# Kernel optimization log

Measured on AMD Instinct MI355X. Metric: run time of the kernel, lower is better.

Reference implementation:

```python
import jax, jax.numpy as jnp
import numpy as np

G = 8          # groups
PATCH = 4      # encoder patch conv kernel/stride
MD = 4         # correlation max displacement -> (2*MD+1)^2 = 81 neighbours
BNEPS = 1e-5
LNEPS = 1e-5

# finite-difference gradient kernel (assumed: forward differences on a C-grid)
GRAD_K = jnp.array([[[[0., 0., 0.], [0., -1., 1.], [0., 0., 0.]]],
                    [[[0., 0., 0.], [0., -1., 0.], [0., 1., 0.]]]], dtype=jnp.float32)

def _vort_kernel():
    # assumed 6x6 Biot-Savart-like vorticity->velocity kernel (CalculusOperators not in source)
    c = 2.5
    ys, xs = np.mgrid[0:6, 0:6].astype(np.float32)
    r2 = (ys - c) ** 2 + (xs - c) ** 2
    u = -(ys - c) / (2.0 * np.pi * r2)
    v = (xs - c) / (2.0 * np.pi * r2)
    return jnp.asarray(np.stack([u, v])[:, None])  # [2,1,6,6]
VORT_K = _vort_kernel()

def conv2d(x, w, pad, stride=1):
    return jax.lax.conv_general_dilated(x, w, (stride, stride), [(pad, pad), (pad, pad)],
                                        dimension_numbers=('NCHW', 'OIHW', 'NCHW'))

def bn(x, g, b):
    # inference-mode BatchNorm with running_mean=0, running_var=1
    return x * (g / jnp.sqrt(1.0 + BNEPS))[None, :, None, None] + b[None, :, None, None]

def up2x(x):
    def lerp_axis(x, axis):
        n = x.shape[axis]
        c = jnp.arange(2 * n, dtype=x.dtype) * (n - 1) / (2 * n - 1)
        i0 = jnp.floor(c).astype(jnp.int32)
        i1 = jnp.minimum(i0 + 1, n - 1)
        w = c - i0.astype(x.dtype)
        a0 = jnp.take(x, i0, axis=axis)
        a1 = jnp.take(x, i1, axis=axis)
        shp = [1] * x.ndim; shp[axis] = 2 * n
        w = w.reshape(shp)
        return a0 * (1 - w) + a1 * w
    return lerp_axis(lerp_axis(x, 2), 3)

def double_conv_up(x, w1, g1, b1, w2, g2, b2):
    x = jax.nn.relu(bn(conv2d(up2x(x), w1, 1), g1, b1))
    return jax.nn.relu(bn(conv2d(up2x(x), w2, 1), g2, b2))

@jax.checkpoint
def correlation(f1, f2):
    # PWC-Net style FunctionCorrelation: mean over channels of f1 * shifted f2, 81 shifts
    N, C, H, W = f1.shape
    f2p = jnp.pad(f2, ((0, 0), (0, 0), (MD, MD), (MD, MD)))
    outs = [jnp.mean(f1 * f2p[:, :, dy:dy + H, dx:dx + W], axis=1)
            for dy in range(2 * MD + 1) for dx in range(2 * MD + 1)]
    return jnp.stack(outs, axis=1)  # [N, 81, H, W]

def cgrid_to_motion(u, v, shape):
    mu = (u[:, :, 1:-1, 1:] + u[:, :, 1:-1, :-1]) * 0.5
    mv = (v[:, :, 1:, 1:-1] + v[:, :, :-1, 1:-1]) * 0.5
    m = jnp.concatenate([mu, mv], axis=1)
    h, w = shape
    up = (m.shape[2] - h) // 2
    left = (m.shape[3] - w) // 2
    return m[:, :, up:up + h, left:left + w]

def calc_phi_velocity(phi, shape):
    vel = conv2d(phi, GRAD_K, 1)
    return cgrid_to_motion(vel[:, 0:1, :, :-1], vel[:, 1:2, :-1, :], shape)

def calc_vort_velocity(stream, shape):
    s = stream[:, :, :-1, :-1]
    vel = conv2d(s, VORT_K, 5)  # full-padding conv == conv_transpose of flipped kernel
    return cgrid_to_motion(vel[:, 0:1, 2:-2, 2:-3], vel[:, 1:2, 2:-3, 2:-2], shape)

def bilinear_sample(f, px, py):
    # f [N,C,H,W]; px,py [N,H,W] absolute coords, border clamp
    H, W = f.shape[-2], f.shape[-1]
    px = jnp.clip(px, 0.0, W - 1.0)
    py = jnp.clip(py, 0.0, H - 1.0)
    x0 = jnp.floor(px); y0 = jnp.floor(py)
    wx = (px - x0)[:, None]; wy = (py - y0)[:, None]
    x0i = x0.astype(jnp.int32); y0i = y0.astype(jnp.int32)
    x1i = jnp.minimum(x0i + 1, W - 1); y1i = jnp.minimum(y0i + 1, H - 1)
    gat = jax.vmap(lambda fi, yi, xi: fi[:, yi, xi])
    v00 = gat(f, y0i, x0i); v01 = gat(f, y0i, x1i)
    v10 = gat(f, y1i, x0i); v11 = gat(f, y1i, x1i)
    return (v00 * (1 - wx) + v01 * wx) * (1 - wy) + (v10 * (1 - wx) + v11 * wx) * wy

def warp(f, vel, sign):
    N, _, H, W = f.shape
    ys, xs = jnp.meshgrid(jnp.arange(H, dtype=f.dtype), jnp.arange(W, dtype=f.dtype), indexing='ij')
    return bilinear_sample(f, xs[None] - sign * vel[:, 0], ys[None] - sign * vel[:, 1])

def bfecc_warp(f, vel):
    f1 = warp(f, vel, 1.0)
    fb = warp(f1, vel, -1.0)
    return warp(f + 0.5 * (f - fb), vel, 1.0)

def _forward(prev, next, texture, mask, boundary,
             enc_w, enc_b,
             phi_w1, phi_g1, phi_b1, phi_w2, phi_g2, phi_b2, phi_ow, phi_ob,
             vor_w1, vor_g1, vor_b1, vor_w2, vor_g2, vor_b2, vor_ow, vor_ob,
             phi_weight, vorticity_weight,
             ln_g, ln_b, fc1_w, fc1_b, fc2_w, fc2_b):
    B, C, H, W = prev.shape
    shape = texture.shape[-2:]
    pm = (prev * mask[:, None]).reshape(B * G, C // G, H, W)
    pb = (prev * boundary[:, None]).reshape(B * G, C // G, H, W)
    nm = (next * mask[:, None]).reshape(B * G, C // G, H, W)
    enc = lambda x: conv2d(x, enc_w, 0, PATCH) + enc_b[None, :, None, None]
    f_nm = enc(nm)
    corr = jnp.concatenate([correlation(enc(pm), f_nm), correlation(enc(pb), f_nm)], axis=1)
    phi = (conv2d(double_conv_up(corr, phi_w1, phi_g1, phi_b1, phi_w2, phi_g2, phi_b2), phi_ow, 0)
           + phi_ob[None, :, None, None]) * phi_weight
    vort = (conv2d(double_conv_up(corr, vor_w1, vor_g1, vor_b1, vor_w2, vor_g2, vor_b2), vor_ow, 0)
            + vor_ob[None, :, None, None]) * vorticity_weight * H
    helm = jnp.concatenate([phi, vort], axis=1)  # [B*G, 2, H, W]
    vel_phi = calc_phi_velocity(helm[:, 0:1], shape)
    vel_vort = calc_vort_velocity(helm[:, 1:2], shape)
    vel = vel_phi + vel_vort
    Bt, Ct, Ht, Wt = texture.shape
    tex = texture.reshape(B * G, Ct // G, Ht, Wt)
    pred = bfecc_warp(tex, vel).reshape(B, Ct, Ht, Wt)
    xp = jnp.transpose(pred, (0, 2, 3, 1))  # [B,H,W,C]
    mu = jnp.mean(xp, -1, keepdims=True)
    var = jnp.var(xp, -1, keepdims=True)
    y = (xp - mu) / jnp.sqrt(var + LNEPS) * ln_g + ln_b
    y = jax.nn.gelu(y @ fc1_w.T + fc1_b, approximate=False)
    y = y @ fc2_w.T + fc2_b
    return pred + jnp.transpose(y, (0, 3, 1, 2))

def setup_inputs():
    ks = jax.random.split(jax.random.key(0), 20)
    B, C, H, W = 4, 64, 260, 260
    Ht, Wt = 258, 258
    D = 128           # correlation_dim
    cg = C // G       # 8 channels per group
    ed = 8            # encoder_dim // groups = 64 // 8
    n = lambda i, shp, s=1.0: jax.random.normal(ks[i], shp, jnp.float32) * s
    return {
        'prev': n(0, (B, C, H, W)), 'next': n(1, (B, C, H, W)),
        'texture': n(2, (B, C, Ht, Wt)),
        'mask': jax.random.uniform(ks[3], (B, H, W), jnp.float32),
        'boundary': jax.random.uniform(ks[4], (B, H, W), jnp.float32),
        'enc_w': n(5, (D, cg, PATCH, PATCH), 0.05), 'enc_b': n(6, (D,), 0.02),
        'phi_w1': n(7, (ed, 162, 3, 3), 0.05), 'phi_g1': jnp.ones(ed), 'phi_b1': jnp.zeros(ed),
        'phi_w2': n(8, (ed, ed, 3, 3), 0.05), 'phi_g2': jnp.ones(ed), 'phi_b2': jnp.zeros(ed),
        'phi_ow': n(9, (1, ed, 1, 1), 0.05), 'phi_ob': n(10, (1,), 0.02),
        'vor_w1': n(11, (ed, 162, 3, 3), 0.05), 'vor_g1': jnp.ones(ed), 'vor_b1': jnp.zeros(ed),
        'vor_w2': n(12, (ed, ed, 3, 3), 0.05), 'vor_g2': jnp.ones(ed), 'vor_b2': jnp.zeros(ed),
        'vor_ow': n(13, (1, ed, 1, 1), 0.05), 'vor_ob': n(14, (1,), 0.02),
        'phi_weight': jnp.array([0.5], jnp.float32),
        'vorticity_weight': jnp.array([0.005], jnp.float32),
        'ln_g': jnp.ones(C), 'ln_b': jnp.zeros(C),
        'fc1_w': n(15, (C, C), 0.05), 'fc1_b': n(16, (C,), 0.02),
        'fc2_w': n(17, (C, C), 0.05), 'fc2_b': n(18, (C,), 0.02),
    }

def reference(prev, next, texture, mask, boundary,
              enc_w, enc_b,
              phi_w1, phi_g1, phi_b1, phi_w2, phi_g2, phi_b2, phi_ow, phi_ob,
              vor_w1, vor_g1, vor_b1, vor_w2, vor_g2, vor_b2, vor_ow, vor_ob,
              phi_weight, vorticity_weight,
              ln_g, ln_b, fc1_w, fc1_b, fc2_w, fc2_b):
    return _forward(prev, next, texture, mask, boundary,
                    enc_w, enc_b,
                    phi_w1, phi_g1, phi_b1, phi_w2, phi_g2, phi_b2, phi_ow, phi_ob,
                    vor_w1, vor_g1, vor_b1, vor_w2, vor_g2, vor_b2, vor_ow, vor_ob,
                    phi_weight, vorticity_weight,
                    ln_g, ln_b, fc1_w, fc1_b, fc2_w, fc2_b)
```

## Files before the change

kernel.cpp:

```cpp
#include <hip/hip_runtime.h>
#include <math.h>


#define NIMG 32
#define HW 260
#define HWT 258
#define EG 65
#define EGP (EG*EG)
#define PIX_T (HWT*HWT)
#define PIX_H (HW*HW)
#define H1N 8652800

__global__ void k_wt(const float* __restrict__ w, float* __restrict__ wt) {
    int e = blockIdx.x * 256 + threadIdx.x;
    if (e < 128 * 128) {
        int d = e >> 7, i = e & 127;
        wt[i * 128 + d] = w[e];
    }
}

__global__ __launch_bounds__(128) void k_enc(
    const float* __restrict__ src,
    const float* __restrict__ mul,
    const float* __restrict__ wt,
    const float* __restrict__ bias,
    float* __restrict__ out)
{
    int xt = blockIdx.x;
    int yo = blockIdx.y;
    int n  = blockIdx.z;
    int bi = n >> 3, g = n & 7;
    int xo0 = xt * 16;
    __shared__ __align__(16) float patch[2048];
    int tid = threadIdx.x;
    const float* sbase = src + (size_t)(bi * 64 + g * 8) * PIX_H;
    const float* mbase = mul + (size_t)bi * PIX_H;
    int row0 = yo * 4, col0 = xo0 * 4;
    for (int e = tid; e < 2048; e += 128) {
        int c = e >> 8, r = (e >> 6) & 3, col = e & 63;
        int gc = col0 + col;
        float v = 0.f;
        if (gc < HW) {
            int off = (row0 + r) * HW + gc;
            v = sbase[(size_t)c * PIX_H + off] * mbase[off];
        }
        patch[e] = v;
    }
    __syncthreads();
    int d = tid;
    float acc[16];
    float bv = bias[d];
#pragma unroll
    for (int p = 0; p < 16; ++p) acc[p] = bv;
    const float4* p4 = (const float4*)patch;
    for (int j = 0; j < 32; ++j) {
        float w0 = wt[(j * 4 + 0) * 128 + d];
        float w1 = wt[(j * 4 + 1) * 128 + d];
        float w2 = wt[(j * 4 + 2) * 128 + d];
        float w3 = wt[(j * 4 + 3) * 128 + d];
#pragma unroll
        for (int p = 0; p < 16; ++p) {
            float4 v = p4[j * 16 + p];
            acc[p] += w0 * v.x + w1 * v.y + w2 * v.z + w3 * v.w;
        }
    }
    size_t ob = ((size_t)(n * EG + yo) * EG + xo0) * 128 + d;
#pragma unroll
    for (int p = 0; p < 16; ++p)
        if (xo0 + p < EG) out[ob + (size_t)p * 128] = acc[p];
}

__global__ __launch_bounds__(128) void k_corr(
    const float* __restrict__ f1,
    const float* __restrict__ f2,
    float* __restrict__ corr,
    int obase)
{
    int bx = blockIdx.x;
    int dy = bx >> 1, xt = bx & 1;
    int y  = blockIdx.y;
    int n  = blockIdx.z;
    int xs = xt ? 33 : 0;
    int nx = xt ? 32 : 33;
    __shared__ __align__(16) float4 s1[33 * 17];
    __shared__ __align__(16) float4 s2[41 * 17];
    int tid = threadIdx.x;
    const float4* g1 = (const float4*)(f1 + ((size_t)(n * EG + y) * EG + xs) * 128);
    int y2 = y + dy - 4;
    bool yok = (y2 >= 0 && y2 < EG);
    const float4* g2 = (const float4*)(f2 + (yok ? ((size_t)(n * EG + y2) * EG) * 128 : 0));
    int q, xl;
    if (xt) { q = tid >> 5; xl = tid & 31; }
    else    { q = tid / 33; xl = tid - q * 33; }
    int dx0 = q * 3;
    bool act = tid < nx * 3;
    float4 a0 = make_float4(0,0,0,0), a1 = a0, a2 = a0;
    for (int half = 0; half < 2; ++half) {
        int cb = half * 16;
        __syncthreads();
        for (int e = tid; e < nx * 16; e += 128) {
            int r = e >> 4, c4 = e & 15;
            s1[r * 17 + c4] = g1[r * 32 + cb + c4];
        }
        for (int e = tid; e < 41 * 16; e += 128) {
            int r = e >> 4, c4 = e & 15;
            int xg = xs - 4 + r;
            float4 v = make_float4(0.f, 0.f, 0.f, 0.f);
            if (yok && xg >= 0 && xg < EG) v = g2[xg * 32 + cb + c4];
            s2[r * 17 + c4] = v;
        }
        __syncthreads();
        if (act) {
            const float4* r1 = s1 + xl * 17;
            const float4* r2 = s2 + (xl + dx0) * 17;
#pragma unroll 8
            for (int i = 0; i < 16; ++i) {
                float4 a = r1[i];
                float4 b0 = r2[i], b1 = r2[17 + i], b2 = r2[34 + i];
                a0.x += a.x * b0.x; a0.y += a.y * b0.y; a0.z += a.z * b0.z; a0.w += a.w * b0.w;
                a1.x += a.x * b1.x; a1.y += a.y * b1.y; a1.z += a.z * b1.z; a1.w += a.w * b1.w;
                a2.x += a.x * b2.x; a2.y += a.y * b2.y; a2.z += a.z * b2.z; a2.w += a.w * b2.w;
            }
        }
    }
    if (act) {
        float s[3];
        s[0] = (a0.x + a0.y + a0.z + a0.w) * (1.0f / 128.0f);
        s[1] = (a1.x + a1.y + a1.z + a1.w) * (1.0f / 128.0f);
        s[2] = (a2.x + a2.y + a2.z + a2.w) * (1.0f / 128.0f);
#pragma unroll
        for (int m = 0; m < 3; ++m) {
            int o = obase + dy * 9 + dx0 + m;
            corr[(size_t)(n * 162 + o) * EGP + y * EG + xs + xl] = s[m];
        }
    }
}

__global__ __launch_bounds__(256) void k_conv1(
    const float* __restrict__ corr,
    const float* __restrict__ w_phi,
    const float* __restrict__ w_vor,
    float* __restrict__ part)
{
    int yp = blockIdx.x;
    int n  = blockIdx.y;
    int zp = blockIdx.z;
    int y0 = yp * 4;
    __shared__ float upc[6 * 6 * 132];
    __shared__ float wch[16 * 6 * 9];
    __shared__ float s_xw[132];
    __shared__ int   s_xi0[132];
    __shared__ int   s_xi1[132];
    __shared__ float s_yw[6];
    __shared__ int   s_yj0[6];
    __shared__ int   s_yj1[6];
    __shared__ int   s_yv[6];
    int tid = threadIdx.x;
    if (tid < 132) {
        int xu = tid - 1;
        if (xu >= 0 && xu <= 129) {
            float cx = (float)(xu * 64) / 129.0f;
            int i0 = (int)cx;
            int i1 = i0 + 1; if (i1 > 64) i1 = 64;
            s_xw[tid] = cx - (float)i0;
            s_xi0[tid] = i0;
            s_xi1[tid] = i1;
        } else { s_xi0[tid] = -1; s_xi1[tid] = 0; s_xw[tid] = 0.f; }
    }
    if (tid >= 132 && tid < 138) {
        int r = tid - 132;
        int yy = y0 - 1 + r;
        if (yy >= 0 && yy <= 129) {
            float cy = (float)(yy * 64) / 129.0f;
            int i0 = (int)cy;
            int i1 = i0 + 1; if (i1 > 64) i1 = 64;
            s_yw[r] = cy - (float)i0;
            s_yj0[r] = i0;
            s_yj1[r] = i1;
            s_yv[r] = 1;
        } else { s_yw[r] = 0.f; s_yj0[r] = 0; s_yj1[r] = 0; s_yv[r] = 0; }
    }
    int og = tid / 26, xg = tid - og * 26;
    int x0 = xg * 5;
    bool act = (og < 8);
    float acc[2][4][5] = {};
    for (int cc = zp * 9; cc < zp * 9 + 9; ++cc) {
        int cb = cc * 6;
        __syncthreads();
        for (int e = tid; e < 4752; e += 256) {
            int r = e / 792, rem = e - r * 792, ci = rem / 132, xx = rem - ci * 132;
            float val = 0.f;
            int xi0 = s_xi0[xx];
            if (s_yv[r] && xi0 >= 0) {
                const float* cp = corr + (size_t)(n * 162 + cb + ci) * EGP;
                int J0 = s_yj0[r] * 65, J1 = s_yj1[r] * 65;
                int xi1 = s_xi1[xx];
                float wxv = s_xw[xx];
                float a0 = __ldg(cp + J0 + xi0), a1 = __ldg(cp + J0 + xi1);
                float b0 = __ldg(cp + J1 + xi0), b1 = __ldg(cp + J1 + xi1);
                float tp = a0 + wxv * (a1 - a0);
                float bt = b0 + wxv * (b1 - b0);
                val = tp + s_yw[r] * (bt - tp);
            }
            upc[e] = val;
        }
        for (int e = tid; e < 864; e += 256) {
            int oc = e / 54, rem = e - oc * 54, ci = rem / 9, k = rem - ci * 9;
            int t2 = oc >> 3, o = oc & 7;
            wch[e] = (t2 ? w_vor : w_phi)[(o * 162 + cb + ci) * 9 + k];
        }
        __syncthreads();
        if (act) {
            for (int ci = 0; ci < 6; ++ci) {
                float wr[2][9];
#pragma unroll
                for (int p = 0; p < 2; ++p)
#pragma unroll
                    for (int k = 0; k < 9; ++k)
                        wr[p][k] = wch[((og + 8 * p) * 6 + ci) * 9 + k];
#pragma unroll
                for (int r = 0; r < 6; ++r) {
                    float u7[7];
                    const float* up = &upc[(r * 6 + ci) * 132 + x0];
#pragma unroll
                    for (int m = 0; m < 7; ++m) u7[m] = up[m];
#pragma unroll
                    for (int ky = 0; ky < 3; ++ky) {
                        int yi = r - ky;
                        if (yi < 0 || yi > 3) continue;
#pragma unroll
                        for (int p = 0; p < 2; ++p)
#pragma unroll
                            for (int kx = 0; kx < 3; ++kx) {
                                float w = wr[p][ky * 3 + kx];
#pragma unroll
                                for (int xi = 0; xi < 5; ++xi)
                                    acc[p][yi][xi] += w * u7[xi + kx];
                            }
                    }
                }
            }
        }
    }
    if (act) {
        float* pbuf = part + (size_t)zp * H1N;
#pragma unroll
        for (int p = 0; p < 2; ++p) {
            size_t pb = (size_t)((p * 32 + n) * 8 + og) * 16900;
#pragma unroll
            for (int yi = 0; yi < 4; ++yi) {
                int row = y0 + yi;
                if (row < 130) {
#pragma unroll
                    for (int xi = 0; xi < 5; ++xi)
                        pbuf[pb + (size_t)row * 130 + (x0 + xi)] = acc[p][yi][xi];
                }
            }
        }
    }
}

__global__ __launch_bounds__(256) void k_h1red(
    const float* __restrict__ part,
    const float* __restrict__ g_phi, const float* __restrict__ b_phi,
    const float* __restrict__ g_vor, const float* __restrict__ b_vor,
    float* __restrict__ h1)
{
    int i4 = blockIdx.x * 256 + threadIdx.x;
    if (i4 >= H1N / 4) return;
    size_t i = (size_t)i4 * 4;
    int c2 = (int)(i / 16900);
    int o = c2 & 7, t2 = c2 >> 8;
    const float bnsc = 1.0f / sqrtf(1.0f + 1e-5f);
    float gsc = (t2 ? g_vor[o] : g_phi[o]) * bnsc;
    float bia = (t2 ? b_vor[o] : b_phi[o]);
    const float4* p0 = (const float4*)(part);
    const float4* p1 = (const float4*)(part + H1N);
    const float4* p2 = (const float4*)(part + 2 * (size_t)H1N);
    float4 a = p0[i4], b = p1[i4], c = p2[i4];
    float4 r;
    r.x = fmaxf((a.x + b.x + c.x) * gsc + bia, 0.f);
    r.y = fmaxf((a.y + b.y + c.y) * gsc + bia, 0.f);
    r.z = fmaxf((a.z + b.z + c.z) * gsc + bia, 0.f);
    r.w = fmaxf((a.w + b.w + c.w) * gsc + bia, 0.f);
    ((float4*)h1)[i4] = r;
}

__global__ __launch_bounds__(256) void k_conv2(
    const float* __restrict__ h1,
    const float* __restrict__ w_phi2, const float* __restrict__ w_vor2,
    const float* __restrict__ g_phi2, const float* __restrict__ b_phi2,
    const float* __restrict__ g_vor2, const float* __restrict__ b_vor2,
    const float* __restrict__ ow_phi, const float* __restrict__ ob_phi,
    const float* __restrict__ ow_vor, const float* __restrict__ ob_vor,
    const float* __restrict__ phi_weight, const float* __restrict__ vort_weight,
    float* __restrict__ helm)
{
    int y = blockIdx.x, n = blockIdx.y;
    __shared__ float hraw[8320];
    __shared__ float wch[1152];
    __shared__ float bns[16], bnb[16], owv[16], obv[2], wm[2];
    int tid = threadIdx.x;
    int ylo = y - 1; if (ylo < 0) ylo = 0;
    int R0 = (int)((float)(ylo * 129) / 259.0f);
    for (int e = tid; e < 8320; e += 256) {
        int t2 = e / 4160, rem = e - t2 * 4160;
        int j = rem / 1040, rem2 = rem - j * 1040;
        int ci = rem2 / 130, xx = rem2 - ci * 130;
        int R = R0 + j; if (R > 129) R = 129;
        hraw[e] = h1[(size_t)((t2 * 32 + n) * 8 + ci) * 16900 + R * 130 + xx];
    }
    for (int e = tid; e < 1152; e += 256) {
        int t2 = e / 576, rem = e - t2 * 576;
        int o = rem / 72, rem2 = rem - o * 72;
        int ci = rem2 / 9, k = rem2 - ci * 9;
        wch[e] = (t2 ? w_vor2 : w_phi2)[(o * 8 + ci) * 9 + k];
    }
    if (tid < 16) {
        int t2 = tid >> 3, o = tid & 7;
        bns[tid] = (t2 ? g_vor2[o] : g_phi2[o]) * (1.0f / sqrtf(1.0f + 1e-5f));
        bnb[tid] = (t2 ? b_vor2[o] : b_phi2[o]);
        owv[tid] = (t2 ? ow_vor[o] : ow_phi[o]);
    }
    if (tid == 0) {
        obv[0] = ob_phi[0]; obv[1] = ob_vor[0];
        wm[0] = phi_weight[0]; wm[1] = vort_weight[0] * 260.0f;
    }
    __syncthreads();
    for (int x = tid; x < HW; x += 256) {
        float wy[3]; int rj0[3], rj1[3]; bool vy[3];
#pragma unroll
        for (int ky = 0; ky < 3; ++ky) {
            int yy = y - 1 + ky;
            vy[ky] = (yy >= 0 && yy < HW);
            if (vy[ky]) {
                float cy = (float)(yy * 129) / 259.0f;
                int i0 = (int)cy; wy[ky] = cy - (float)i0;
                int i1 = i0 + 1; if (i1 > 129) i1 = 129;
                rj0[ky] = i0 - R0; rj1[ky] = i1 - R0;
            } else { wy[ky] = 0; rj0[ky] = 0; rj1[ky] = 0; }
        }
        float wxv[3]; int c0[3], c1[3]; bool vx[3];
#pragma unroll
        for (int kx = 0; kx < 3; ++kx) {
            int xxp = x - 1 + kx;
            vx[kx] = (xxp >= 0 && xxp < HW);
            if (vx[kx]) {
                float cx = (float)(xxp * 129) / 259.0f;
                int i0 = (int)cx; wxv[kx] = cx - (float)i0;
                int i1 = i0 + 1; if (i1 > 129) i1 = 129;
                c0[kx] = i0; c1[kx] = i1;
            } else { wxv[kx] = 0; c0[kx] = 0; c1[kx] = 0; }
        }
        float res[2];
#pragma unroll
        for (int t2 = 0; t2 < 2; ++t2) {
            float acc[8] = {0,0,0,0,0,0,0,0};
            for (int ci = 0; ci < 8; ++ci) {
#pragma unroll
                for (int ky = 0; ky < 3; ++ky) {
                    if (!vy[ky]) continue;
                    const float* r0p = &hraw[((t2 * 4 + rj0[ky]) * 8 + ci) * 130];
                    const float* r1p = &hraw[((t2 * 4 + rj1[ky]) * 8 + ci) * 130];
                    float u3[3];
#pragma unroll
                    for (int kx = 0; kx < 3; ++kx) {
                        if (vx[kx]) {
                            float tp = r0p[c0[kx]] + wxv[kx] * (r0p[c1[kx]] - r0p[c0[kx]]);
                            float bt = r1p[c0[kx]] + wxv[kx] * (r1p[c1[kx]] - r1p[c0[kx]]);
                            u3[kx] = tp + wy[ky] * (bt - tp);
                        } else u3[kx] = 0.f;
                    }
#pragma unroll
                    for (int o = 0; o < 8; ++o) {
                        const float* wp = &wch[((t2 * 8 + o) * 8 + ci) * 9 + ky * 3];
                        acc[o] += wp[0] * u3[0] + wp[1] * u3[1] + wp[2] * u3[2];
                    }
                }
            }
            float dot = 0.f;
#pragma unroll
            for (int o = 0; o < 8; ++o) {
                float hv = fmaxf(acc[o] * bns[t2 * 8 + o] + bnb[t2 * 8 + o], 0.f);
                dot += owv[t2 * 8 + o] * hv;
            }
            res[t2] = (dot + obv[t2]) * wm[t2];
        }
        helm[(size_t)(n * 2 + 0) * PIX_H + y * HW + x] = res[0];
        helm[(size_t)(n * 2 + 1) * PIX_H + y * HW + x] = res[1];
    }
}

__device__ __forceinline__ float K0f(int a, int b) {
    if (a < 0 || a > 5 || b < 0 || b > 5) return 0.f;
    float fa = (float)a - 2.5f, fb = (float)b - 2.5f;
    float r2 = fa * fa + fb * fb;
    return -fa / (6.28318530717958647692f * r2);
}
__device__ __forceinline__ float K1f(int a, int b) {
    if (a < 0 || a > 5 || b < 0 || b > 5) return 0.f;
    float fa = (float)a - 2.5f, fb = (float)b - 2.5f;
    float r2 = fa * fa + fb * fb;
    return fb / (6.28318530717958647692f * r2);
}

__global__ __launch_bounds__(256) void k_vel(
    const float* __restrict__ helm, float* __restrict__ vel)
{
    int idx = blockIdx.x * 256 + threadIdx.x;
    if (idx >= NIMG * PIX_T) return;
    int n = idx / PIX_T, pix = idx - n * PIX_T;
    int yy = pix / HWT, xx = pix - yy * HWT;
    const float* phi = helm + (size_t)(n * 2) * PIX_H;
    const float* s   = helm + (size_t)(n * 2 + 1) * PIX_H;
    float sv[7][7];
#pragma unroll
    for (int di = 0; di < 7; ++di) {
        int i = yy + di - 3;
#pragma unroll
        for (int dj = 0; dj < 7; ++dj) {
            int j = xx + dj - 3;
            sv[di][dj] = (i >= 0 && i < 259 && j >= 0 && j < 259) ? s[i * HW + j] : 0.f;
        }
    }
    float ax = 0.5f * (phi[(yy + 1) * HW + xx + 2] - phi[(yy + 1) * HW + xx]);
#pragma unroll
    for (int a = 0; a < 6; ++a)
#pragma unroll
        for (int d = 0; d < 7; ++d) {
            float coef = K0f(a, d) + K0f(a, d - 1);
            ax += 0.5f * coef * sv[a + 1][d];
        }
    float ay = 0.5f * (phi[(yy + 2) * HW + xx + 1] - phi[yy * HW + xx + 1]);
#pragma unroll
    for (int d = 0; d < 7; ++d)
#pragma unroll
        for (int b = 0; b < 6; ++b) {
            float coef = K1f(d, b) + K1f(d - 1, b);
            ay += 0.5f * coef * sv[d][b + 1];
        }
    vel[(size_t)(n * 2) * PIX_T + pix]     = ax;
    vel[(size_t)(n * 2 + 1) * PIX_T + pix] = ay;
}

__device__ __forceinline__ float bsample(const float* __restrict__ plane,
                                         float px, float py) {
    px = fminf(fmaxf(px, 0.f), 257.f);
    py = fminf(fmaxf(py, 0.f), 257.f);
    float fx = floorf(px), fy = floorf(py);
    int x0 = (int)fx, y0 = (int)fy;
    float wx = px - fx, wy = py - fy;
    int x1 = x0 + 1; if (x1 > 257) x1 = 257;
    int y1 = y0 + 1; if (y1 > 257) y1 = 257;
    const float* r0 = plane + y0 * HWT;
    const float* r1 = plane + y1 * HWT;
    float v00 = r0[x0], v01 = r0[x1], v10 = r1[x0], v11 = r1[x1];
    float tp = v00 + wx * (v01 - v00);
    float bt = v10 + wx * (v11 - v10);
    return tp + wy * (bt - tp);
}

__global__ __launch_bounds__(256) void k_warp(
    const float* __restrict__ src,
    const float* __restrict__ vel,
    float sign,
    const float* __restrict__ tex,
    int mode,
    float* __restrict__ out)
{
    int idx = blockIdx.x * 256 + threadIdx.x;
    if (idx >= NIMG * 8 * PIX_T) return;
    int plane_i = idx / PIX_T;
    int pix = idx - plane_i * PIX_T;
    int n = plane_i >> 3;
    int y = pix / HWT, x = pix - y * HWT;
    float vx = vel[(size_t)(n * 2) * PIX_T + pix];
    float vy = vel[(size_t)(n * 2 + 1) * PIX_T + pix];
    const float* plane = src + (size_t)plane_i * PIX_T;
    float v = bsample(plane, (float)x - sign * vx, (float)y - sign * vy);
    if (mode) v = 1.5f * tex[idx] - 0.5f * v;
    out[idx] = v;
}

__global__ __launch_bounds__(256, 2) void k_lnmlp(
    float* __restrict__ out,
    const float* __restrict__ lng, const float* __restrict__ lnb,
    const float* __restrict__ w1, const float* __restrict__ b1,
    const float* __restrict__ w2, const float* __restrict__ b2)
{
    int yy = blockIdx.x, b = blockIdx.y;
    __shared__ __align__(16) float sw1[4096];
    __shared__ __align__(16) float sw2t[4096];
    __shared__ float sb1[64], sb2[64], sg[64], sbt[64];
    int tid = threadIdx.x;
    for (int e = tid; e < 4096; e += 256) {
        sw1[e] = w1[e];
        sw2t[(e & 63) * 64 + (e >> 6)] = w2[e];
    }
    if (tid < 64) { sb1[tid] = b1[tid]; sb2[tid] = b2[tid]; sg[tid] = lng[tid]; sbt[tid] = lnb[tid]; }
    __syncthreads();
    float* base = out + (size_t)b * 64 * PIX_T + (size_t)yy * HWT;
    for (int x = tid; x < HWT; x += 256) {
        float sum = 0.f, sumsq = 0.f;
        for (int k = 0; k < 64; ++k) {
            float v = base[(size_t)k * PIX_T + x];
            sum += v; sumsq += v * v;
        }
        float mu = sum * (1.0f / 64.0f);
        float var = sumsq * (1.0f / 64.0f) - mu * mu;
        float inv = 1.0f / sqrtf(var + 1e-5f);
        float xn[64];
#pragma unroll
        for (int k = 0; k < 64; ++k) {
            float v = base[(size_t)k * PIX_T + x];
            xn[k] = (v - mu) * inv * sg[k] + sbt[k];
        }
        float acc2[64];
#pragma unroll
        for (int j2 = 0; j2 < 64; ++j2) acc2[j2] = 0.f;
        for (int j = 0; j < 64; ++j) {
            float t = sb1[j];
            const float4* wrow = (const float4*)&sw1[j * 64];
#pragma unroll
            for (int k4 = 0; k4 < 16; ++k4) {
                float4 w = wrow[k4];
                t += xn[4 * k4] * w.x + xn[4 * k4 + 1] * w.y
                   + xn[4 * k4 + 2] * w.z + xn[4 * k4 + 3] * w.w;
            }
            float hj = 0.5f * t * (1.0f + erff(t * 0.70710678118654752f));
            const float4* w2row = (const float4*)&sw2t[j * 64];
#pragma unroll
            for (int q = 0; q < 16; ++q) {
                float4 w = w2row[q];
                acc2[4 * q]     += hj * w.x;
                acc2[4 * q + 1] += hj * w.y;
                acc2[4 * q + 2] += hj * w.z;
                acc2[4 * q + 3] += hj * w.w;
            }
        }
#pragma unroll
        for (int j2 = 0; j2 < 64; ++j2)
            base[(size_t)j2 * PIX_T + x] += sb2[j2] + acc2[j2];
    }
}

extern "C" void kernel_launch(void* const* d_in, const int* in_sizes, int n_in,
                              void* d_out, int out_size, void* d_ws, size_t ws_size,
                              hipStream_t stream) {
    const float* prev       = (const float*)d_in[0];
    const float* next       = (const float*)d_in[1];
    const float* texture    = (const float*)d_in[2];
    const float* mask       = (const float*)d_in[3];
    const float* boundary   = (const float*)d_in[4];
    const float* enc_w      = (const float*)d_in[5];
    const float* enc_b      = (const float*)d_in[6];
    const float* phi_w1     = (const float*)d_in[7];
    const float* phi_g1     = (const float*)d_in[8];
    const float* phi_b1     = (const float*)d_in[9];
    const float* phi_w2     = (const float*)d_in[10];
    const float* phi_g2     = (const float*)d_in[11];
    const float* phi_b2     = (const float*)d_in[12];
    const float* phi_ow     = (const float*)d_in[13];
    const float* phi_ob     = (const float*)d_in[14];
    const float* vor_w1     = (const float*)d_in[15];
    const float* vor_g1     = (const float*)d_in[16];
    const float* vor_b1     = (const float*)d_in[17];
    const float* vor_w2     = (const float*)d_in[18];
    const float* vor_g2     = (const float*)d_in[19];
    const float* vor_b2     = (const float*)d_in[20];
    const float* vor_ow     = (const float*)d_in[21];
    const float* vor_ob     = (const float*)d_in[22];
    const float* phi_weight = (const float*)d_in[23];
    const float* vor_weight = (const float*)d_in[24];
    const float* ln_g       = (const float*)d_in[25];
    const float* ln_b       = (const float*)d_in[26];
    const float* fc1_w      = (const float*)d_in[27];
    const float* fc1_b      = (const float*)d_in[28];
    const float* fc2_w      = (const float*)d_in[29];
    const float* fc2_b      = (const float*)d_in[30];

    float* ws = (float*)d_ws;
    float* F_NM = ws + 0;
    float* F_A  = ws + 17305600;
    float* CORR = ws + 34611200;
    float* WT   = ws + 56513600;
    float* PART = ws + 0;
    float* H1   = ws + 25958400;
    float* HELM = ws + 17305600;
    float* VEL  = ws + 21632000;
    float* F1B  = ws + 34611200;
    float* F2B  = ws + 0;
    float* OUT  = (float*)d_out;

    k_wt<<<dim3(64), dim3(256), 0, stream>>>(enc_w, WT);

    dim3 encg(5, 65, 32);
    k_enc<<<encg, dim3(128), 0, stream>>>(next, mask, WT, enc_b, F_NM);
    k_enc<<<encg, dim3(128), 0, stream>>>(prev, mask, WT, enc_b, F_A);

    dim3 corrg(18, 65, 32);
    k_corr<<<corrg, dim3(128), 0, stream>>>(F_A, F_NM, CORR, 0);
    k_enc<<<encg, dim3(128), 0, stream>>>(prev, boundary, WT, enc_b, F_A);
    k_corr<<<corrg, dim3(128), 0, stream>>>(F_A, F_NM, CORR, 81);

    k_conv1<<<dim3(33, 32, 3), dim3(256), 0, stream>>>(
        CORR, phi_w1, vor_w1, PART);
    k_h1red<<<dim3((H1N / 4 + 255) / 256), dim3(256), 0, stream>>>(
        PART, phi_g1, phi_b1, vor_g1, vor_b1, H1);

    k_conv2<<<dim3(260, 32), dim3(256), 0, stream>>>(
        H1, phi_w2, vor_w2, phi_g2, phi_b2, vor_g2, vor_b2,
        phi_ow, phi_ob, vor_ow, vor_ob, phi_weight, vor_weight, HELM);

    int nv = NIMG * PIX_T;
    k_vel<<<dim3((nv + 255) / 256), dim3(256), 0, stream>>>(HELM, VEL);

    int nw = NIMG * 8 * PIX_T;
    int wb = (nw + 255) / 256;
    k_warp<<<dim3(wb), dim3(256), 0, stream>>>(texture, VEL,  1.0f, texture, 0, F1B);
    k_warp<<<dim3(wb), dim3(256), 0, stream>>>(F1B,     VEL, -1.0f, texture, 1, F2B);
    k_warp<<<dim3(wb), dim3(256), 0, stream>>>(F2B,     VEL,  1.0f, texture, 0, OUT);

    k_lnmlp<<<dim3(258, 4), dim3(256), 0, stream>>>(
        OUT, ln_g, ln_b, fc1_w, fc1_b, fc2_w, fc2_b);
}
```

Measured before the change: 2.839 ms.

## Retile conv1 into four channel splits with 320 threads; read corr f1 directly

In k_conv1, the input-channel reduction is split four ways instead of three, and each block now runs 320 threads. Each thread computes 4 output columns instead of 5, using a float4 plus float2 load from a 136-padded shared row, and the precomputed row offsets and x index arrays are simplified. k_corr drops its shared-memory staging of f1 and reads each thread's own f1 row straight from global memory. Workspace buffers are remapped, with H1 placed in the output buffer, so the fourth partial-sum slice fits, and k_h1red now sums four partials. The intent is higher occupancy and parallelism in the conv1 stage, at the cost of extra partial-sum traffic and uncoalesced per-thread global reads in k_corr.

```diff
diff --git a/kernel.cpp b/kernel.cpp
--- a/kernel.cpp
+++ b/kernel.cpp
@@ -82,10 +82,8 @@
     int n  = blockIdx.z;
     int xs = xt ? 33 : 0;
     int nx = xt ? 32 : 33;
-    __shared__ __align__(16) float4 s1[33 * 17];
     __shared__ __align__(16) float4 s2[41 * 17];
     int tid = threadIdx.x;
-    const float4* g1 = (const float4*)(f1 + ((size_t)(n * EG + y) * EG + xs) * 128);
     int y2 = y + dy - 4;
     bool yok = (y2 >= 0 && y2 < EG);
     const float4* g2 = (const float4*)(f2 + (yok ? ((size_t)(n * EG + y2) * EG) * 128 : 0));
@@ -94,14 +92,11 @@
     else    { q = tid / 33; xl = tid - q * 33; }
     int dx0 = q * 3;
     bool act = tid < nx * 3;
+    const float4* g1 = (const float4*)(f1 + ((size_t)(n * EG + y) * EG + xs + xl) * 128);
     float4 a0 = make_float4(0,0,0,0), a1 = a0, a2 = a0;
     for (int half = 0; half < 2; ++half) {
         int cb = half * 16;
         __syncthreads();
-        for (int e = tid; e < nx * 16; e += 128) {
-            int r = e >> 4, c4 = e & 15;
-            s1[r * 17 + c4] = g1[r * 32 + cb + c4];
-        }
         for (int e = tid; e < 41 * 16; e += 128) {
             int r = e >> 4, c4 = e & 15;
             int xg = xs - 4 + r;
@@ -111,11 +106,10 @@
         }
         __syncthreads();
         if (act) {
-            const float4* r1 = s1 + xl * 17;
             const float4* r2 = s2 + (xl + dx0) * 17;
-#pragma unroll 8
+#pragma unroll
             for (int i = 0; i < 16; ++i) {
-                float4 a = r1[i];
+                float4 a = g1[cb + i];
                 float4 b0 = r2[i], b1 = r2[17 + i], b2 = r2[34 + i];
                 a0.x += a.x * b0.x; a0.y += a.y * b0.y; a0.z += a.z * b0.z; a0.w += a.w * b0.w;
                 a1.x += a.x * b1.x; a1.y += a.y * b1.y; a1.z += a.z * b1.z; a1.w += a.w * b1.w;
@@ -136,7 +130,7 @@
     }
 }
 
-__global__ __launch_bounds__(256) void k_conv1(
+__global__ __launch_bounds__(320) void k_conv1(
     const float* __restrict__ corr,
     const float* __restrict__ w_phi,
     const float* __restrict__ w_vor,
@@ -146,97 +140,99 @@
     int n  = blockIdx.y;
     int zp = blockIdx.z;
     int y0 = yp * 4;
-    __shared__ float upc[6 * 6 * 132];
-    __shared__ float wch[16 * 6 * 9];
-    __shared__ float s_xw[132];
-    __shared__ int   s_xi0[132];
-    __shared__ int   s_xi1[132];
+    __shared__ __align__(16) float upc[36 * 136];
+    __shared__ float wch[16 * 54];
+    __shared__ float s_xw[136];
+    __shared__ int   s_xi0[136];
     __shared__ float s_yw[6];
     __shared__ int   s_yj0[6];
     __shared__ int   s_yj1[6];
     __shared__ int   s_yv[6];
     int tid = threadIdx.x;
-    if (tid < 132) {
+    if (tid < 136) {
         int xu = tid - 1;
         if (xu >= 0 && xu <= 129) {
             float cx = (float)(xu * 64) / 129.0f;
             int i0 = (int)cx;
-            int i1 = i0 + 1; if (i1 > 64) i1 = 64;
             s_xw[tid] = cx - (float)i0;
             s_xi0[tid] = i0;
-            s_xi1[tid] = i1;
-        } else { s_xi0[tid] = -1; s_xi1[tid] = 0; s_xw[tid] = 0.f; }
-    }
-    if (tid >= 132 && tid < 138) {
-        int r = tid - 132;
+        } else { s_xi0[tid] = -1; s_xw[tid] = 0.f; }
+    }
+    if (tid >= 136 && tid < 142) {
+        int r = tid - 136;
         int yy = y0 - 1 + r;
         if (yy >= 0 && yy <= 129) {
             float cy = (float)(yy * 64) / 129.0f;
             int i0 = (int)cy;
             int i1 = i0 + 1; if (i1 > 64) i1 = 64;
             s_yw[r] = cy - (float)i0;
-            s_yj0[r] = i0;
-            s_yj1[r] = i1;
+            s_yj0[r] = i0 * 65;
+            s_yj1[r] = i1 * 65;
             s_yv[r] = 1;
         } else { s_yw[r] = 0.f; s_yj0[r] = 0; s_yj1[r] = 0; s_yv[r] = 0; }
     }
-    int og = tid / 26, xg = tid - og * 26;
-    int x0 = xg * 5;
+    int og = tid / 33, xg = tid - og * 33;
+    int x0 = xg * 4;
     bool act = (og < 8);
-    float acc[2][4][5] = {};
-    for (int cc = zp * 9; cc < zp * 9 + 9; ++cc) {
+    float acc[2][4][4] = {};
+    int cc0 = zp * 7;
+    int cc1 = cc0 + 7; if (cc1 > 27) cc1 = 27;
+    for (int cc = cc0; cc < cc1; ++cc) {
         int cb = cc * 6;
+        const float* cbase = corr + (size_t)(n * 162 + cb) * EGP;
         __syncthreads();
-        for (int e = tid; e < 4752; e += 256) {
-            int r = e / 792, rem = e - r * 792, ci = rem / 132, xx = rem - ci * 132;
+        for (int e = tid; e < 4896; e += 320) {
+            int r = e / 816, rem = e - r * 816;
+            int ci = rem / 136, xx = rem - ci * 136;
             float val = 0.f;
             int xi0 = s_xi0[xx];
             if (s_yv[r] && xi0 >= 0) {
-                const float* cp = corr + (size_t)(n * 162 + cb + ci) * EGP;
-                int J0 = s_yj0[r] * 65, J1 = s_yj1[r] * 65;
-                int xi1 = s_xi1[xx];
+                const float* cp = cbase + ci * EGP;
                 float wxv = s_xw[xx];
-                float a0 = __ldg(cp + J0 + xi0), a1 = __ldg(cp + J0 + xi1);
-                float b0 = __ldg(cp + J1 + xi0), b1 = __ldg(cp + J1 + xi1);
+                int i0a = s_yj0[r] + xi0;
+                int i0b = s_yj1[r] + xi0;
+                float a0 = cp[i0a], a1 = cp[i0a + 1];
+                float b0 = cp[i0b], b1 = cp[i0b + 1];
                 float tp = a0 + wxv * (a1 - a0);
                 float bt = b0 + wxv * (b1 - b0);
                 val = tp + s_yw[r] * (bt - tp);
             }
             upc[e] = val;
         }
-        for (int e = tid; e < 864; e += 256) {
-            int oc = e / 54, rem = e - oc * 54, ci = rem / 9, k = rem - ci * 9;
+        for (int e = tid; e < 864; e += 320) {
+            int oc = e / 54, rem = e - oc * 54;
             int t2 = oc >> 3, o = oc & 7;
-            wch[e] = (t2 ? w_vor : w_phi)[(o * 162 + cb + ci) * 9 + k];
+            wch[e] = (t2 ? w_vor : w_phi)[(o * 162 + cb) * 9 + rem];
         }
         __syncthreads();
         if (act) {
             for (int ci = 0; ci < 6; ++ci) {
-                float wr[2][9];
-#pragma unroll
-                for (int p = 0; p < 2; ++p)
-#pragma unroll
-                    for (int k = 0; k < 9; ++k)
-                        wr[p][k] = wch[((og + 8 * p) * 6 + ci) * 9 + k];
+                float wr0[9], wr1[9];
+#pragma unroll
+                for (int k = 0; k < 9; ++k) {
+                    wr0[k] = wch[og * 54 + ci * 9 + k];
+                    wr1[k] = wch[(og + 8) * 54 + ci * 9 + k];
+                }
 #pragma unroll
                 for (int r = 0; r < 6; ++r) {
-                    float u7[7];
-                    const float* up = &upc[(r * 6 + ci) * 132 + x0];
-#pragma unroll
-                    for (int m = 0; m < 7; ++m) u7[m] = up[m];
+                    const float* up = &upc[(r * 6 + ci) * 136 + x0];
+                    float4 u4 = *(const float4*)up;
+                    float2 u2 = *(const float2*)(up + 4);
+                    float u[6] = {u4.x, u4.y, u4.z, u4.w, u2.x, u2.y};
 #pragma unroll
                     for (int ky = 0; ky < 3; ++ky) {
                         int yi = r - ky;
                         if (yi < 0 || yi > 3) continue;
 #pragma unroll
-                        for (int p = 0; p < 2; ++p)
-#pragma unroll
-                            for (int kx = 0; kx < 3; ++kx) {
-                                float w = wr[p][ky * 3 + kx];
-#pragma unroll
-                                for (int xi = 0; xi < 5; ++xi)
-                                    acc[p][yi][xi] += w * u7[xi + kx];
+                        for (int kx = 0; kx < 3; ++kx) {
+                            float w0 = wr0[ky * 3 + kx];
+                            float w1 = wr1[ky * 3 + kx];
+#pragma unroll
+                            for (int xi = 0; xi < 4; ++xi) {
+                                acc[0][yi][xi] += w0 * u[xi + kx];
+                                acc[1][yi][xi] += w1 * u[xi + kx];
                             }
+                        }
                     }
                 }
             }
@@ -252,8 +248,11 @@
                 int row = y0 + yi;
                 if (row < 130) {
 #pragma unroll
-                    for (int xi = 0; xi < 5; ++xi)
-                        pbuf[pb + (size_t)row * 130 + (x0 + xi)] = acc[p][yi][xi];
+                    for (int xi = 0; xi < 4; ++xi) {
+                        int col = x0 + xi;
+                        if (col < 130)
+                            pbuf[pb + (size_t)row * 130 + col] = acc[p][yi][xi];
+                    }
                 }
             }
         }
@@ -275,14 +274,15 @@
     float gsc = (t2 ? g_vor[o] : g_phi[o]) * bnsc;
     float bia = (t2 ? b_vor[o] : b_phi[o]);
     const float4* p0 = (const float4*)(part);
-    const float4* p1 = (const float4*)(part + H1N);
+    const float4* p1 = (const float4*)(part + (size_t)H1N);
     const float4* p2 = (const float4*)(part + 2 * (size_t)H1N);
-    float4 a = p0[i4], b = p1[i4], c = p2[i4];
+    const float4* p3 = (const float4*)(part + 3 * (size_t)H1N);
+    float4 a = p0[i4], b = p1[i4], c = p2[i4], d = p3[i4];
     float4 r;
-    r.x = fmaxf((a.x + b.x + c.x) * gsc + bia, 0.f);
-    r.y = fmaxf((a.y + b.y + c.y) * gsc + bia, 0.f);
-    r.z = fmaxf((a.z + b.z + c.z) * gsc + bia, 0.f);
-    r.w = fmaxf((a.w + b.w + c.w) * gsc + bia, 0.f);
+    r.x = fmaxf((a.x + b.x + c.x + d.x) * gsc + bia, 0.f);
+    r.y = fmaxf((a.y + b.y + c.y + d.y) * gsc + bia, 0.f);
+    r.z = fmaxf((a.z + b.z + c.z + d.z) * gsc + bia, 0.f);
+    r.w = fmaxf((a.w + b.w + c.w + d.w) * gsc + bia, 0.f);
     ((float4*)h1)[i4] = r;
 }
 
@@ -585,11 +585,11 @@
     float* CORR = ws + 34611200;
     float* WT   = ws + 56513600;
     float* PART = ws + 0;
-    float* H1   = ws + 25958400;
-    float* HELM = ws + 17305600;
-    float* VEL  = ws + 21632000;
+    float* H1   = (float*)d_out;
+    float* HELM = ws + 0;
+    float* VEL  = ws + 4326400;
     float* F1B  = ws + 34611200;
-    float* F2B  = ws + 0;
+    float* F2B  = ws + 8652800;
     float* OUT  = (float*)d_out;
 
     k_wt<<<dim3(64), dim3(256), 0, stream>>>(enc_w, WT);
@@ -603,7 +603,7 @@
     k_enc<<<encg, dim3(128), 0, stream>>>(prev, boundary, WT, enc_b, F_A);
     k_corr<<<corrg, dim3(128), 0, stream>>>(F_A, F_NM, CORR, 81);
 
-    k_conv1<<<dim3(33, 32, 3), dim3(256), 0, stream>>>(
+    k_conv1<<<dim3(33, 32, 4), dim3(320), 0, stream>>>(
         CORR, phi_w1, vor_w1, PART);
     k_h1red<<<dim3((H1N / 4 + 255) / 256), dim3(256), 0, stream>>>(
         PART, phi_g1, phi_b1, vor_g1, vor_b1, H1);
```

New measurement: 3.554 ms. 1.25x slower.
